# Performance work log

Hardware: AMD Instinct MI355X
Metric: run time of the kernel (lower is better)

## Reference

```python
import jax, jax.numpy as jnp
import numpy as np

N_NODES = 500_000
N_EDGES = 8_000_000
N_GRAPHS = 1000


def _mlp(x, w1, b1, w2, b2):
    # Linear -> SELU -> Linear (torch Sequential equivalent)
    return jax.nn.selu(x @ w1 + b1) @ w2 + b2


def setup_inputs() -> dict:
    key = jax.random.key(0)
    ks = jax.random.split(key, 25)
    p = lambda i, shape: jax.random.normal(ks[i], shape, jnp.float32) * 0.1
    return {
        "nodes": jax.random.normal(ks[0], (N_NODES, 1), jnp.float32),
        "edges": jax.random.normal(ks[1], (N_EDGES, 1), jnp.float32),
        "senders": jax.random.randint(ks[2], (N_EDGES,), 0, N_NODES),
        "receivers": jax.random.randint(ks[3], (N_EDGES,), 0, N_NODES),
        "graph_ids": jnp.sort(jax.random.randint(ks[4], (N_NODES,), 0, N_GRAPHS)),
        "num_graphs": N_GRAPHS,
        # permutate_nodes: 2 -> 10 -> 10
        "pn_w1": p(5, (2, 10)), "pn_b1": p(6, (10,)), "pn_w2": p(7, (10, 10)), "pn_b2": p(8, (10,)),
        # update_edges: 11 -> 5 -> 1
        "ue_w1": p(9, (11, 5)), "ue_b1": p(10, (5,)), "ue_w2": p(11, (5, 1)), "ue_b2": p(12, (1,)),
        # permutate_edges: 1 -> 5 -> 10
        "pe_w1": p(13, (1, 5)), "pe_b1": p(14, (5,)), "pe_w2": p(15, (5, 10)), "pe_b2": p(16, (10,)),
        # update_nodes: 11 -> 5 -> 1
        "un_w1": p(17, (11, 5)), "un_b1": p(18, (5,)), "un_w2": p(19, (5, 1)), "un_b2": p(20, (1,)),
        # predict: 11 -> 10 -> 10
        "pr_w1": p(21, (11, 10)), "pr_b1": p(22, (10,)), "pr_w2": p(23, (10, 10)), "pr_b2": p(24, (10,)),
    }


def reference(nodes, edges, pn_w1, pn_b1, pn_w2, pn_b2,
              ue_w1, ue_b1, ue_w2, ue_b2,
              pe_w1, pe_b1, pe_w2, pe_b2,
              un_w1, un_b1, un_w2, un_b2,
              pr_w1, pr_b1, pr_w2, pr_b2,
              senders, receivers, graph_ids, num_graphs):
    # gather node feats to edges: [recv || send] -> (E, 2)
    collected = jnp.concatenate([nodes[receivers], nodes[senders]], axis=-1)
    h1_nodes = _mlp(collected, pn_w1, pn_b1, pn_w2, pn_b2)  # (E, 10)
    h1_edges = edges  # (E, 1)
    for _ in range(3):
        h1_edges = _mlp(jnp.concatenate([h1_edges, h1_nodes], axis=-1),
                        ue_w1, ue_b1, ue_w2, ue_b2)  # (E, 1)
    # edges -> nodes aggregation (sum over receiver)
    edges_of_nodes = jax.ops.segment_sum(h1_edges, receivers, num_segments=nodes.shape[0])  # (N, 1)
    h2_edges = _mlp(edges_of_nodes, pe_w1, pe_b1, pe_w2, pe_b2)  # (N, 10)
    h2_nodes = nodes  # (N, 1)
    for _ in range(3):
        h2_nodes = _mlp(jnp.concatenate([h2_nodes, h2_edges], axis=-1),
                        un_w1, un_b1, un_w2, un_b2)  # (N, 1)
    # nodes -> globals aggregation (sum per graph)
    g = jax.ops.segment_sum(jnp.concatenate([h2_nodes, h2_edges], axis=-1),
                            graph_ids, num_segments=num_graphs)  # (G, 11)
    out = _mlp(g, pr_w1, pr_b1, pr_w2, pr_b2)  # (G, 10)
    return jax.nn.softmax(out, axis=-1)
```

## Files before the change

kernel.cpp:

```cpp
#include <hip/hip_runtime.h>
#include <hip/hip_fp16.h>
#include <math.h>

#define N_NODES_C  500000
#define N_EDGES_C  8000000
#define N_GRAPHS_C 1000
#define NGROUPS_C  (N_EDGES_C / 4)

#define BSHIFT  11
#define BWIDTH  2048
#define NBKT    245

#define PART_TPB 512
#define EPB     16384
#define GPB     (EPB / 4)
#define NPB     ((NGROUPS_C + GPB - 1) / GPB)
#define SROW    496
#define RITER   (GPB / PART_TPB)

#define P2_TPB  512
#define EPB2    8192
#define GPB2    (EPB2 / 4)
#define NPB2    ((NGROUPS_C + GPB2 - 1) / GPB2)
#define SROW2   992
#define RITER2  (GPB2 / P2_TPB)

#define GRAPH_ACC_OFF 0
#define PARTIALS_OFF  11008
#define FW_OFF        33024
#define ZERO_HEAD     33024

#define STARTS_OFF    33280
#define PAIRS_OFF     (STARTS_OFF + 246 * SROW)
#define WS_WORDS_NEEDED (PAIRS_OFF + NPB * EPB)

#define STARTS2_OFF   33280
#define PAIRS64_OFF   (STARTS2_OFF + 246 * SROW2)
#define WS2_WORDS_NEEDED (PAIRS64_OFF + NPB2 * EPB2 * 2)

#define OLD_NODE_ACC_OFF 33536
#define OLD_ZERO_WORDS   (OLD_NODE_ACC_OFF + N_NODES_C)

#define LOG2E_F 1.4426950408889634f


__device__ __forceinline__ float selu2(float xl) {
    const float C1 = 0.7282901039f;
    const float C2 = 1.7580993408473766f;
    float e = __builtin_amdgcn_exp2f(xl);
    float neg = fmaf(C2, e, -C2);
    return xl > 0.0f ? C1 * xl : neg;
}

__device__ __forceinline__ float selu_f(float x) {
    const float scale = 1.0507009873554805f;
    const float sa    = 1.0507009873554805f * 1.6732632423543772f;
    float neg = sa * (__expf(x) - 1.0f);
    return x > 0.0f ? scale * x : neg;
}

__device__ __forceinline__ void atomAddF(float* p, float v) {
    __hip_atomic_fetch_add(p, v, __ATOMIC_RELAXED, __HIP_MEMORY_SCOPE_AGENT);
}

__device__ __forceinline__ void fuse_weights(
        int t,
        const float* __restrict__ pn_w1, const float* __restrict__ pn_b1,
        const float* __restrict__ pn_w2, const float* __restrict__ pn_b2,
        const float* __restrict__ ue_w1, const float* __restrict__ ue_b1,
        const float* __restrict__ ue_w2, const float* __restrict__ ue_b2,
        const float* __restrict__ pe_w1, const float* __restrict__ pe_b1,
        const float* __restrict__ pe_w2, const float* __restrict__ pe_b2,
        const float* __restrict__ un_w1, const float* __restrict__ un_b1,
        const float* __restrict__ un_w2, const float* __restrict__ un_b2,
        float* __restrict__ fw) {
    const float L = LOG2E_F;
    if (t < 20) fw[0 + t] = pn_w1[t] * L;
    if (t < 10) fw[20 + t] = pn_b1[t] * L;
    if (t < 50) {
        int j = t / 5, k = t % 5;
        float s = 0.0f;
        for (int m = 0; m < 10; ++m) s += pn_w2[j * 10 + m] * ue_w1[(1 + m) * 5 + k];
        fw[30 + t] = s * L;
    }
    if (t < 5) {
        float s = ue_b1[t];
        for (int m = 0; m < 10; ++m) s += pn_b2[m] * ue_w1[(1 + m) * 5 + t];
        fw[80 + t] = s * L;
    }
    if (t < 5)  fw[85 + t]  = ue_w1[t] * L;
    if (t < 5)  fw[90 + t]  = ue_w2[t];
    if (t == 0) fw[95]      = ue_b2[0];
    if (t < 5)  fw[96 + t]  = pe_w1[t] * L;
    if (t < 5)  fw[101 + t] = pe_b1[t] * L;
    if (t < 50) fw[106 + t] = pe_w2[t];
    if (t < 10) fw[156 + t] = pe_b2[t];
    if (t < 25) {
        int j = t / 5, k = t % 5;
        float s = 0.0f;
        for (int m = 0; m < 10; ++m) s += pe_w2[j * 10 + m] * un_w1[(1 + m) * 5 + k];
        fw[166 + t] = s * L;
    }
    if (t < 5) {
        float s = un_b1[t];
        for (int m = 0; m < 10; ++m) s += pe_b2[m] * un_w1[(1 + m) * 5 + t];
        fw[191 + t] = s * L;
    }
    if (t < 5)  fw[196 + t] = un_w1[t] * L;
    if (t < 5)  fw[201 + t] = un_w2[t];
    if (t == 0) fw[206]     = un_b2[0];
}

__global__ __launch_bounds__(256) void k_init(
        float* __restrict__ ws,
        const float* pn_w1, const float* pn_b1, const float* pn_w2, const float* pn_b2,
        const float* ue_w1, const float* ue_b1, const float* ue_w2, const float* ue_b2,
        const float* pe_w1, const float* pe_b1, const float* pe_w2, const float* pe_b2,
        const float* un_w1, const float* un_b1, const float* un_w2, const float* un_b2) {
    int i = blockIdx.x * 256 + threadIdx.x;
    if (i < ZERO_HEAD) ws[i] = 0.0f;
    if (blockIdx.x == 0)
        fuse_weights(threadIdx.x, pn_w1, pn_b1, pn_w2, pn_b2, ue_w1, ue_b1, ue_w2, ue_b2,
                     pe_w1, pe_b1, pe_w2, pe_b2, un_w1, un_b1, un_w2, un_b2, ws + FW_OFF);
}

__global__ void k_fuse(const float* pn_w1, const float* pn_b1, const float* pn_w2, const float* pn_b2,
                       const float* ue_w1, const float* ue_b1, const float* ue_w2, const float* ue_b2,
                       const float* pe_w1, const float* pe_b1, const float* pe_w2, const float* pe_b2,
                       const float* un_w1, const float* un_b1, const float* un_w2, const float* un_b2,
                       float* fw) {
    fuse_weights(threadIdx.x, pn_w1, pn_b1, pn_w2, pn_b2, ue_w1, ue_b1, ue_w2, ue_b2,
                 pe_w1, pe_b1, pe_w2, pe_b2, un_w1, un_b1, un_w2, un_b2, fw);
}

__global__ void k_final(const float* __restrict__ graph_acc,
                        const float* __restrict__ partials,
                        const float* __restrict__ pr_w1, const float* __restrict__ pr_b1,
                        const float* __restrict__ pr_w2, const float* __restrict__ pr_b2,
                        float* __restrict__ out) {
    int g = blockIdx.x * blockDim.x + threadIdx.x;
    if (g >= N_GRAPHS_C) return;
    float gv[11];
#pragma unroll
    for (int f = 0; f < 11; ++f)
        gv[f] = graph_acc[g * 11 + f] + partials[g * 11 + f] + partials[11000 + g * 11 + f];
    float h[10];
#pragma unroll
    for (int j = 0; j < 10; ++j) {
        float z = pr_b1[j];
#pragma unroll
        for (int f = 0; f < 11; ++f) z = fmaf(gv[f], pr_w1[f * 10 + j], z);
        h[j] = selu_f(z);
    }
    float o[10];
    float mx = -1e30f;
#pragma unroll
    for (int j = 0; j < 10; ++j) {
        float z = pr_b2[j];
#pragma unroll
        for (int m = 0; m < 10; ++m) z = fmaf(h[m], pr_w2[m * 10 + j], z);
        o[j] = z;
        mx = fmaxf(mx, z);
    }
    float sum = 0.0f;
#pragma unroll
    for (int j = 0; j < 10; ++j) { o[j] = __expf(o[j] - mx); sum += o[j]; }
    float inv = 1.0f / sum;
#pragma unroll
    for (int j = 0; j < 10; ++j) out[g * 10 + j] = o[j] * inv;
}


__global__ __launch_bounds__(P2_TPB) void k_part2(
        const float* __restrict__ edges,
        const int* __restrict__ senders, const int* __restrict__ receivers,
        int* __restrict__ starts_T, unsigned long long* __restrict__ pairs64) {
    __shared__ int hist[256];
    __shared__ int cursorS[256];
    __shared__ alignas(16) unsigned long long staged[EPB2];

    int tid = threadIdx.x;
    int p   = blockIdx.x;
    int gstart = p * GPB2;
    int gnum   = NGROUPS_C - gstart;
    if (gnum > GPB2) gnum = GPB2;

    if (tid < 256) hist[tid] = 0;
    __syncthreads();

    int4 rv4[RITER2];
#pragma unroll
    for (int r = 0; r < RITER2; ++r) {
        int idx = r * P2_TPB + tid;
        int gi  = gstart + (idx < gnum ? idx : 0);
        rv4[r] = ((const int4*)receivers)[gi];
        if (idx < gnum) {
            atomicAdd(&hist[rv4[r].x >> BSHIFT], 1);
            atomicAdd(&hist[rv4[r].y >> BSHIFT], 1);
            atomicAdd(&hist[rv4[r].z >> BSHIFT], 1);
            atomicAdd(&hist[rv4[r].w >> BSHIFT], 1);
        }
    }
    __syncthreads();

    int orig = 0, val = 0;
    if (tid < 256) { orig = hist[tid]; val = orig; }
    for (int d = 1; d < 256; d <<= 1) {
        int add = 0;
        if (tid >= d && tid < 256) add = hist[tid - d];
        __syncthreads();
        if (tid >= d && tid < 256) { val += add; hist[tid] = val; }
        __syncthreads();
    }
    int excl = val - orig;
    if (tid < 256) cursorS[tid] = excl;
    if (tid < 246) starts_T[tid * SROW2 + p] = excl;
    __syncthreads();

#pragma unroll
    for (int r = 0; r < RITER2; ++r) {
        int idx = r * P2_TPB + tid;
        int gi  = gstart + (idx < gnum ? idx : 0);
        float4 e4 = ((const float4*)edges)[gi];
        int4   s4 = ((const int4*)senders)[gi];
        int4   rv = rv4[r];
        if (idx < gnum) {
            int   rvv[4] = {rv.x, rv.y, rv.z, rv.w};
            int   svv[4] = {s4.x, s4.y, s4.z, s4.w};
            float evv[4] = {e4.x, e4.y, e4.z, e4.w};
#pragma unroll
            for (int u = 0; u < 4; ++u) {
                int bkt  = rvv[u] >> BSHIFT;
                int slot = atomicAdd(&cursorS[bkt], 1);
                unsigned long long pk =
                    ((unsigned long long)(rvv[u] & (BWIDTH - 1)) << 51)
                  | ((unsigned long long)(unsigned)svv[u] << 32)
                  | (unsigned long long)__float_as_uint(evv[u]);
                staged[slot] = pk;
            }
        }
    }
    __syncthreads();

    const uint4* st4 = (const uint4*)staged;
    uint4* dst = (uint4*)(pairs64 + (size_t)p * EPB2);
    int n4 = gnum * 2;
    for (int i = tid; i < n4; i += P2_TPB) dst[i] = st4[i];
}

__global__ __launch_bounds__(1024) void k_gather2(
        const float* __restrict__ nodes, const int* __restrict__ graph_ids,
        const float* __restrict__ fw, const int* __restrict__ starts_T,
        const unsigned long long* __restrict__ pairs64,
        float* __restrict__ graph_acc, float* __restrict__ partials) {
    __shared__ float accf[BWIDTH];
    __shared__ float nf[BWIDTH];
    __shared__ int   s0[NPB2];
    __shared__ int   pst[NPB2 + 1];
    __shared__ int   sc[1024];
    __shared__ float garr[32 * 11];
    int tid = threadIdx.x;
    int b   = blockIdx.x;

    int nodeBase = b << BSHIFT;
    int lastIdx  = nodeBase + BWIDTH;
    if (lastIdx > N_NODES_C) lastIdx = N_NODES_C;
    int lim = lastIdx - nodeBase;

    accf[tid] = 0.0f; accf[1024 + tid] = 0.0f;
    nf[tid]        = (tid        < lim) ? nodes[nodeBase + tid]        : 0.0f;
    nf[1024 + tid] = (1024 + tid < lim) ? nodes[nodeBase + 1024 + tid] : 0.0f;
    if (tid < 352) garr[tid] = 0.0f;

    int cntv = 0;
    if (tid < NPB2) {
        int a = starts_T[b * SROW2 + tid];
        int c = starts_T[(b + 1) * SROW2 + tid];
        s0[tid] = a;
        cntv = c - a;
    }
    sc[tid] = cntv;
    __syncthreads();

    int v = cntv;
    for (int d = 1; d < 1024; d <<= 1) {
        int add = (tid >= d) ? sc[tid - d] : 0;
        __syncthreads();
        if (tid >= d) { v += add; sc[tid] = v; }
        __syncthreads();
    }
    if (tid == 0) pst[0] = 0;
    if (tid < NPB2) pst[tid + 1] = v;
    __syncthreads();

    int M = pst[NPB2];

    {
        float w_pn1[20], b_pn1[10], W_eb[50], b_eb[5], w1r0[5], w2e[5];
#pragma unroll
        for (int j = 0; j < 20; ++j) w_pn1[j] = fw[j];
#pragma unroll
        for (int j = 0; j < 10; ++j) b_pn1[j] = fw[20 + j];
#pragma unroll
        for (int j = 0; j < 50; ++j) W_eb[j] = fw[30 + j];
#pragma unroll
        for (int j = 0; j < 5; ++j) b_eb[j] = fw[80 + j];
#pragma unroll
        for (int j = 0; j < 5; ++j) w1r0[j] = fw[85 + j];
#pragma unroll
        for (int j = 0; j < 5; ++j) w2e[j] = fw[90 + j];
        float b2e = fw[95];

#pragma unroll 1
        for (int i = tid; i < M; i += 1024) {
            int lo = 0, hi = NPB2;
            while (hi - lo > 1) {
                int mid = (lo + hi) >> 1;
                if (pst[mid] <= i) lo = mid; else hi = mid;
            }
            int off = i - pst[lo];
            unsigned long long pk = pairs64[(size_t)lo * EPB2 + s0[lo] + off];
            int   rl   = (int)(pk >> 51);
            int   sidx = (int)((pk >> 32) & 0x7FFFFULL);
            float e    = __uint_as_float((unsigned)pk);
            float nr   = nf[rl];
            float ns   = nodes[sidx];

            float bs[5];
#pragma unroll
            for (int k = 0; k < 5; ++k) bs[k] = b_eb[k];
#pragma unroll
            for (int j = 0; j < 10; ++j) {
                float zl = fmaf(nr, w_pn1[j], fmaf(ns, w_pn1[10 + j], b_pn1[j]));
                float sz = selu2(zl);
#pragma unroll
                for (int k = 0; k < 5; ++k) bs[k] = fmaf(sz, W_eb[j * 5 + k], bs[k]);
            }
#pragma unroll
            for (int it = 0; it < 3; ++it) {
                float acc2 = b2e;
#pragma unroll
                for (int k = 0; k < 5; ++k) {
                    float tt = selu2(fmaf(e, w1r0[k], bs[k]));
                    acc2 = fmaf(tt, w2e[k], acc2);
                }
                e = acc2;
            }
            atomicAdd(&accf[rl], e);
        }
    }
    __syncthreads();

    float w_pe1[5], b_pe1[5], pe_w2[50], pe_b2[10], W_nb[25], b_nb[5], w1r0n[5], w2n[5];
#pragma unroll
    for (int j = 0; j < 5; ++j) w_pe1[j] = fw[96 + j];
#pragma unroll
    for (int j = 0; j < 5; ++j) b_pe1[j] = fw[101 + j];
#pragma unroll
    for (int j = 0; j < 50; ++j) pe_w2[j] = fw[106 + j];
#pragma unroll
    for (int j = 0; j < 10; ++j) pe_b2[j] = fw[156 + j];
#pragma unroll
    for (int j = 0; j < 25; ++j) W_nb[j] = fw[166 + j];
#pragma unroll
    for (int j = 0; j < 5; ++j) b_nb[j] = fw[191 + j];
#pragma unroll
    for (int j = 0; j < 5; ++j) w1r0n[j] = fw[196 + j];
#pragma unroll
    for (int j = 0; j < 5; ++j) w2n[j] = fw[201 + j];
    float b2n = fw[206];

    int gidBase = graph_ids[nodeBase];
    int gidEnd  = graph_ids[lastIdx - 1];

#pragma unroll
    for (int q = 0; q < 2; ++q) {
        int local = q * 1024 + tid;
        int i = nodeBase + local;
        bool valid = i < N_NODES_C;

        float s = accf[local];
        float t5[5];
#pragma unroll
        for (int k = 0; k < 5; ++k) t5[k] = selu2(fmaf(s, w_pe1[k], b_pe1[k]));
        float he[10];
#pragma unroll
        for (int m = 0; m < 10; ++m) {
            float a = pe_b2[m];
#pragma unroll
            for (int k = 0; k < 5; ++k) a = fmaf(t5[k], pe_w2[k * 10 + m], a);
            he[m] = a;
        }
        float bs[5];
#pragma unroll
        for (int k = 0; k < 5; ++k) {
            float a = b_nb[k];
#pragma unroll
            for (int t = 0; t < 5; ++t) a = fmaf(t5[t], W_nb[t * 5 + k], a);
            bs[k] = a;
        }
        float n = valid ? nf[local] : 0.0f;
#pragma unroll
        for (int it = 0; it < 3; ++it) {
            float a = b2n;
#pragma unroll
            for (int k = 0; k < 5; ++k) {
                float tt = selu2(fmaf(n, w1r0n[k], bs[k]));
                a = fmaf(tt, w2n[k], a);
            }
            n = a;
        }

        int gid = valid ? graph_ids[i] : -1;
        if (!valid) {
            n = 0.0f;
#pragma unroll
            for (int m = 0; m < 10; ++m) he[m] = 0.0f;
        }

        int gid0 = __shfl(gid, 0, 64);
        bool allsame = __all(gid == gid0) && (gid0 >= 0);
        if (allsame) {
            float vv = n;
#pragma unroll
            for (int off = 32; off > 0; off >>= 1) vv += __shfl_down(vv, off, 64);
            float vh[10];
#pragma unroll
            for (int m = 0; m < 10; ++m) {
                float ww = he[m];
#pragma unroll
                for (int off = 32; off > 0; off >>= 1) ww += __shfl_down(ww, off, 64);
                vh[m] = ww;
            }
            if ((tid & 63) == 0) {
                int off = gid0 - gidBase;
                if (off >= 0 && off < 32) {
                    atomicAdd(&garr[off * 11 + 0], vv);
#pragma unroll
                    for (int m = 0; m < 10; ++m) atomicAdd(&garr[off * 11 + 1 + m], vh[m]);
                } else {
                    atomAddF(&graph_acc[gid0 * 11 + 0], vv);
#pragma unroll
                    for (int m = 0; m < 10; ++m) atomAddF(&graph_acc[gid0 * 11 + 1 + m], vh[m]);
                }
            }
        } else if (valid) {
            int off = gid - gidBase;
            if (off >= 0 && off < 32) {
                atomicAdd(&garr[off * 11 + 0], n);
#pragma unroll
                for (int m = 0; m < 10; ++m) atomicAdd(&garr[off * 11 + 1 + m], he[m]);
            } else {
                atomAddF(&graph_acc[gid * 11 + 0], n);
#pragma unroll
                for (int m = 0; m < 10; ++m) atomAddF(&graph_acc[gid * 11 + 1 + m], he[m]);
            }
        }
    }
    __syncthreads();

    int ngl = gidEnd - gidBase + 1;
    if (ngl > 32) ngl = 32;
    int par = (b & 1) * 11000;
    for (int t = tid; t < ngl * 11; t += 1024) {
        int off = t / 11, f = t - off * 11;
        partials[par + (gidBase + off) * 11 + f] = garr[t];
    }
}


__global__ __launch_bounds__(PART_TPB, 4) void k_part(
        const float* __restrict__ nodes, const float* __restrict__ edges,
        const int* __restrict__ senders, const int* __restrict__ receivers,
        const float* __restrict__ fw, int* __restrict__ starts_T,
        unsigned int* __restrict__ pairs) {
    __shared__ int hist[256];
    __shared__ int cursorS[256];
    __shared__ unsigned int staged[EPB];

    int tid = threadIdx.x;
    int p   = blockIdx.x;
    int gstart = p * GPB;
    int gnum   = NGROUPS_C - gstart;
    if (gnum > GPB) gnum = GPB;

    float w_pn1[20], b_pn1[10], W_eb[50], b_eb[5], w1r0[5], w2e[5];
#pragma unroll
    for (int j = 0; j < 20; ++j) w_pn1[j] = fw[j];
#pragma unroll
    for (int j = 0; j < 10; ++j) b_pn1[j] = fw[20 + j];
#pragma unroll
    for (int j = 0; j < 50; ++j) W_eb[j] = fw[30 + j];
#pragma unroll
    for (int j = 0; j < 5; ++j) b_eb[j] = fw[80 + j];
#pragma unroll
    for (int j = 0; j < 5; ++j) w1r0[j] = fw[85 + j];
#pragma unroll
    for (int j = 0; j < 5; ++j) w2e[j] = fw[90 + j];
    float b2e = fw[95];

    if (tid < 256) hist[tid] = 0;
    __syncthreads();

#pragma unroll 1
    for (int r = 0; r < RITER; ++r) {
        int idx = r * PART_TPB + tid;
        int gi  = gstart + (idx < gnum ? idx : 0);
        int4 rv = ((const int4*)receivers)[gi];
        if (idx < gnum) {
            atomicAdd(&hist[rv.x >> BSHIFT], 1);
            atomicAdd(&hist[rv.y >> BSHIFT], 1);
            atomicAdd(&hist[rv.z >> BSHIFT], 1);
            atomicAdd(&hist[rv.w >> BSHIFT], 1);
        }
    }
    __syncthreads();

    int orig = 0, val = 0;
    if (tid < 256) { orig = hist[tid]; val = orig; }
    for (int d = 1; d < 256; d <<= 1) {
        int add = 0;
        if (tid >= d && tid < 256) add = hist[tid - d];
        __syncthreads();
        if (tid >= d && tid < 256) { val += add; hist[tid] = val; }
        __syncthreads();
    }
    int excl = val - orig;
    if (tid < 256) cursorS[tid] = excl;
    if (tid < 246) starts_T[tid * SROW + p] = excl;
    __syncthreads();

    float4 e4A, e4B, e4N;
    int4   s4A, s4B, s4N, r4A, r4B, r4N;
    float  nsA0, nsA1, nsA2, nsA3, nrA0, nrA1, nrA2, nrA3;
    float  nsB0, nsB1, nsB2, nsB3, nrB0, nrB1, nrB2, nrB3;

    {
        int gi0 = gstart + (tid < gnum ? tid : 0);
        e4A = ((const float4*)edges)[gi0];
        s4A = ((const int4*)senders)[gi0];
        r4A = ((const int4*)receivers)[gi0];
        nsA0 = nodes[s4A.x]; nsA1 = nodes[s4A.y];
        nsA2 = nodes[s4A.z]; nsA3 = nodes[s4A.w];
        nrA0 = nodes[r4A.x]; nrA1 = nodes[r4A.y];
        nrA2 = nodes[r4A.z]; nrA3 = nodes[r4A.w];
        int idx1 = PART_TPB + tid;
        int gi1 = gstart + (idx1 < gnum ? idx1 : 0);
        e4B = ((const float4*)edges)[gi1];
        s4B = ((const int4*)senders)[gi1];
        r4B = ((const int4*)receivers)[gi1];
    }

#pragma unroll 1
    for (int r = 0; r < RITER; ++r) {
        {
            int idx2 = (r + 2) * PART_TPB + tid;
            int gi2  = gstart + (idx2 < gnum ? idx2 : 0);
            e4N = ((const float4*)edges)[gi2];
            s4N = ((const int4*)senders)[gi2];
            r4N = ((const int4*)receivers)[gi2];
        }
        nsB0 = nodes[s4B.x]; nsB1 = nodes[s4B.y];
        nsB2 = nodes[s4B.z]; nsB3 = nodes[s4B.w];
        nrB0 = nodes[r4B.x]; nrB1 = nodes[r4B.y];
        nrB2 = nodes[r4B.z]; nrB3 = nodes[r4B.w];

        float ev[4]  = {e4A.x, e4A.y, e4A.z, e4A.w};
        int   rv[4]  = {r4A.x, r4A.y, r4A.z, r4A.w};
        float nsv[4] = {nsA0, nsA1, nsA2, nsA3};
        float nrv[4] = {nrA0, nrA1, nrA2, nrA3};

        bool validr = (r * PART_TPB + tid) < gnum;
#pragma unroll
        for (int u = 0; u < 4; ++u) {
            float nr = nrv[u], ns = nsv[u];
            float bs[5];
#pragma unroll
            for (int k = 0; k < 5; ++k) bs[k] = b_eb[k];
#pragma unroll
            for (int j = 0; j < 10; ++j) {
                float zl = fmaf(nr, w_pn1[j], fmaf(ns, w_pn1[10 + j], b_pn1[j]));
                float sz = selu2(zl);
#pragma unroll
                for (int k = 0; k < 5; ++k) bs[k] = fmaf(sz, W_eb[j * 5 + k], bs[k]);
            }
            float e = ev[u];
#pragma unroll
            for (int it = 0; it < 3; ++it) {
                float acc2 = b2e;
#pragma unroll
                for (int k = 0; k < 5; ++k) {
                    float tt = selu2(fmaf(e, w1r0[k], bs[k]));
                    acc2 = fmaf(tt, w2e[k], acc2);
                }
                e = acc2;
            }
            if (validr) {
                int bkt  = rv[u] >> BSHIFT;
                int slot = atomicAdd(&cursorS[bkt], 1);
                unsigned int pk = ((unsigned int)(rv[u] & (BWIDTH - 1)) << 16)
                                | (unsigned int)__half_as_ushort(__float2half_rn(e));
                staged[slot] = pk;
            }
        }

        e4A = e4B; s4A = s4B; r4A = r4B;
        nsA0 = nsB0; nsA1 = nsB1; nsA2 = nsB2; nsA3 = nsB3;
        nrA0 = nrB0; nrA1 = nrB1; nrA2 = nrB2; nrA3 = nrB3;
        e4B = e4N; s4B = s4N; r4B = r4N;
    }
    __syncthreads();

    const uint4* staged4 = (const uint4*)staged;
    uint4* dst = (uint4*)(pairs + (size_t)p * EPB);
    for (int i = tid; i < gnum; i += PART_TPB) dst[i] = staged4[i];
}

__global__ __launch_bounds__(1024) void k_gather(
        const float* __restrict__ nodes, const int* __restrict__ graph_ids,
        const float* __restrict__ fw, const int* __restrict__ starts_T,
        const unsigned int* __restrict__ pairs, float* __restrict__ graph_acc,
        float* __restrict__ partials) {
    __shared__ float accf[BWIDTH];
    __shared__ int s0[SROW], s1[SROW];
    __shared__ float garr[32 * 11];
    int tid = threadIdx.x;
    int b   = blockIdx.x;

    accf[tid] = 0.0f; accf[1024 + tid] = 0.0f;
    if (tid < 352) garr[tid] = 0.0f;
    for (int i = tid; i < NPB; i += 1024) {
        s0[i] = starts_T[b * SROW + i];
        s1[i] = starts_T[(b + 1) * SROW + i];
    }
    __syncthreads();

    int g32 = tid >> 5, lane = tid & 31;
    for (int p = g32; p < NPB; p += 32) {
        int st = s0[p], en = s1[p];
        const unsigned int* seg = pairs + (size_t)p * EPB + st;
        int cnt = en - st;
        for (int i = lane; i < cnt; i += 32) {
            unsigned int pk = seg[i];
            atomicAdd(&accf[(pk >> 16) & (BWIDTH - 1)],
                      __half2float(__ushort_as_half((unsigned short)(pk & 0xffff))));
        }
    }
    __syncthreads();

    float w_pe1[5], b_pe1[5], pe_w2[50], pe_b2[10], W_nb[25], b_nb[5], w1r0n[5], w2n[5];
#pragma unroll
    for (int j = 0; j < 5; ++j) w_pe1[j] = fw[96 + j];
#pragma unroll
    for (int j = 0; j < 5; ++j) b_pe1[j] = fw[101 + j];
#pragma unroll
    for (int j = 0; j < 50; ++j) pe_w2[j] = fw[106 + j];
#pragma unroll
    for (int j = 0; j < 10; ++j) pe_b2[j] = fw[156 + j];
#pragma unroll
    for (int j = 0; j < 25; ++j) W_nb[j] = fw[166 + j];
#pragma unroll
    for (int j = 0; j < 5; ++j) b_nb[j] = fw[191 + j];
#pragma unroll
    for (int j = 0; j < 5; ++j) w1r0n[j] = fw[196 + j];
#pragma unroll
    for (int j = 0; j < 5; ++j) w2n[j] = fw[201 + j];
    float b2n = fw[206];

    int nodeBase = b << BSHIFT;
    int lastIdx  = nodeBase + BWIDTH;
    if (lastIdx > N_NODES_C) lastIdx = N_NODES_C;
    int gidBase = graph_ids[nodeBase];
    int gidEnd  = graph_ids[lastIdx - 1];

#pragma unroll
    for (int q = 0; q < 2; ++q) {
        int local = q * 1024 + tid;
        int i = nodeBase + local;
        bool valid = i < N_NODES_C;

        float s = accf[local];
        float t5[5];
#pragma unroll
        for (int k = 0; k < 5; ++k) t5[k] = selu2(fmaf(s, w_pe1[k], b_pe1[k]));
        float he[10];
#pragma unroll
        for (int m = 0; m < 10; ++m) {
            float a = pe_b2[m];
#pragma unroll
            for (int k = 0; k < 5; ++k) a = fmaf(t5[k], pe_w2[k * 10 + m], a);
            he[m] = a;
        }
        float bs[5];
#pragma unroll
        for (int k = 0; k < 5; ++k) {
            float a = b_nb[k];
#pragma unroll
            for (int t = 0; t < 5; ++t) a = fmaf(t5[t], W_nb[t * 5 + k], a);
            bs[k] = a;
        }
        float n = valid ? nodes[i] : 0.0f;
#pragma unroll
        for (int it = 0; it < 3; ++it) {
            float a = b2n;
#pragma unroll
            for (int k = 0; k < 5; ++k) {
                float tt = selu2(fmaf(n, w1r0n[k], bs[k]));
                a = fmaf(tt, w2n[k], a);
            }
            n = a;
        }

        int gid = valid ? graph_ids[i] : -1;
        if (!valid) {
            n = 0.0f;
#pragma unroll
            for (int m = 0; m < 10; ++m) he[m] = 0.0f;
        }

        int gid0 = __shfl(gid, 0, 64);
        bool allsame = __all(gid == gid0) && (gid0 >= 0);
        if (allsame) {
            float v = n;
#pragma unroll
            for (int off = 32; off > 0; off >>= 1) v += __shfl_down(v, off, 64);
            float vh[10];
#pragma unroll
            for (int m = 0; m < 10; ++m) {
                float ww = he[m];
#pragma unroll
                for (int off = 32; off > 0; off >>= 1) ww += __shfl_down(ww, off, 64);
                vh[m] = ww;
            }
            if ((tid & 63) == 0) {
                int off = gid0 - gidBase;
                if (off >= 0 && off < 32) {
                    atomicAdd(&garr[off * 11 + 0], v);
#pragma unroll
                    for (int m = 0; m < 10; ++m) atomicAdd(&garr[off * 11 + 1 + m], vh[m]);
                } else {
                    atomAddF(&graph_acc[gid0 * 11 + 0], v);
#pragma unroll
                    for (int m = 0; m < 10; ++m) atomAddF(&graph_acc[gid0 * 11 + 1 + m], vh[m]);
                }
            }
        } else if (valid) {
            int off = gid - gidBase;
            if (off >= 0 && off < 32) {
                atomicAdd(&garr[off * 11 + 0], n);
#pragma unroll
                for (int m = 0; m < 10; ++m) atomicAdd(&garr[off * 11 + 1 + m], he[m]);
            } else {
                atomAddF(&graph_acc[gid * 11 + 0], n);
#pragma unroll
                for (int m = 0; m < 10; ++m) atomAddF(&graph_acc[gid * 11 + 1 + m], he[m]);
            }
        }
    }
    __syncthreads();

    int ngl = gidEnd - gidBase + 1;
    if (ngl > 32) ngl = 32;
    int par = (b & 1) * 11000;
    for (int t = tid; t < ngl * 11; t += 1024) {
        int off = t / 11, f = t - off * 11;
        partials[par + (gidBase + off) * 11 + f] = garr[t];
    }
}


__global__ __launch_bounds__(256) void k_zero(float* __restrict__ ws, int len4) {
    int i = blockIdx.x * 256 + threadIdx.x;
    if (i < len4) ((float4*)ws)[i] = make_float4(0.f, 0.f, 0.f, 0.f);
}

__global__ __launch_bounds__(256) void k_edges(
        const float* __restrict__ nodes, const float* __restrict__ edges,
        const int* __restrict__ senders, const int* __restrict__ receivers,
        const float* __restrict__ fw, float* __restrict__ node_acc) {
    float w_pn1[20], b_pn1[10], W_eb[50], b_eb[5], w1r0[5], w2e[5];
#pragma unroll
    for (int j = 0; j < 20; ++j) w_pn1[j] = fw[j];
#pragma unroll
    for (int j = 0; j < 10; ++j) b_pn1[j] = fw[20 + j];
#pragma unroll
    for (int j = 0; j < 50; ++j) W_eb[j] = fw[30 + j];
#pragma unroll
    for (int j = 0; j < 5; ++j) b_eb[j] = fw[80 + j];
#pragma unroll
    for (int j = 0; j < 5; ++j) w1r0[j] = fw[85 + j];
#pragma unroll
    for (int j = 0; j < 5; ++j) w2e[j] = fw[90 + j];
    float b2e = fw[95];

    int g = blockIdx.x * 256 + threadIdx.x;
    if (g >= NGROUPS_C) return;

    float4 e4 = ((const float4*)edges)[g];
    int4  s4 = ((const int4*)senders)[g];
    int4  r4 = ((const int4*)receivers)[g];
    float ev[4] = {e4.x, e4.y, e4.z, e4.w};
    int   sv[4] = {s4.x, s4.y, s4.z, s4.w};
    int   rv[4] = {r4.x, r4.y, r4.z, r4.w};
    float nsv[4], nrv[4];
#pragma unroll
    for (int u = 0; u < 4; ++u) { nsv[u] = nodes[sv[u]]; nrv[u] = nodes[rv[u]]; }
#pragma unroll
    for (int u = 0; u < 4; ++u) {
        float nr = nrv[u], ns = nsv[u];
        float bs[5];
#pragma unroll
        for (int k = 0; k < 5; ++k) bs[k] = b_eb[k];
#pragma unroll
        for (int j = 0; j < 10; ++j) {
            float zl = fmaf(nr, w_pn1[j], fmaf(ns, w_pn1[10 + j], b_pn1[j]));
            float sz = selu2(zl);
#pragma unroll
            for (int k = 0; k < 5; ++k) bs[k] = fmaf(sz, W_eb[j * 5 + k], bs[k]);
        }
        float e = ev[u];
#pragma unroll
        for (int it = 0; it < 3; ++it) {
            float acc2 = b2e;
#pragma unroll
            for (int k = 0; k < 5; ++k) {
                float tt = selu2(fmaf(e, w1r0[k], bs[k]));
                acc2 = fmaf(tt, w2e[k], acc2);
            }
            e = acc2;
        }
        atomAddF(&node_acc[rv[u]], e);
    }
}

__global__ __launch_bounds__(256) void k_nodes(
        const float* __restrict__ nodes, const int* __restrict__ graph_ids,
        const float* __restrict__ fw, const float* __restrict__ node_acc,
        float* __restrict__ graph_acc) {
    float w_pe1[5], b_pe1[5], pe_w2[50], pe_b2[10], W_nb[25], b_nb[5], w1r0n[5], w2n[5];
#pragma unroll
    for (int j = 0; j < 5; ++j) w_pe1[j] = fw[96 + j];
#pragma unroll
    for (int j = 0; j < 5; ++j) b_pe1[j] = fw[101 + j];
#pragma unroll
    for (int j = 0; j < 50; ++j) pe_w2[j] = fw[106 + j];
#pragma unroll
    for (int j = 0; j < 10; ++j) pe_b2[j] = fw[156 + j];
#pragma unroll
    for (int j = 0; j < 25; ++j) W_nb[j] = fw[166 + j];
#pragma unroll
    for (int j = 0; j < 5; ++j) b_nb[j] = fw[191 + j];
#pragma unroll
    for (int j = 0; j < 5; ++j) w1r0n[j] = fw[196 + j];
#pragma unroll
    for (int j = 0; j < 5; ++j) w2n[j] = fw[201 + j];
    float b2n = fw[206];

    int i = blockIdx.x * 256 + threadIdx.x;
    bool valid = i < N_NODES_C;
    int ii = valid ? i : (N_NODES_C - 1);

    float s = node_acc[ii];
    float t5[5];
#pragma unroll
    for (int k = 0; k < 5; ++k) t5[k] = selu2(fmaf(s, w_pe1[k], b_pe1[k]));
    float he[10];
#pragma unroll
    for (int m = 0; m < 10; ++m) {
        float a = pe_b2[m];
#pragma unroll
        for (int k = 0; k < 5; ++k) a = fmaf(t5[k], pe_w2[k * 10 + m], a);
        he[m] = a;
    }
    float bs[5];
#pragma unroll
    for (int k = 0; k < 5; ++k) {
        float a = b_nb[k];
#pragma unroll
        for (int t = 0; t < 5; ++t) a = fmaf(t5[t], W_nb[t * 5 + k], a);
        bs[k] = a;
    }
    float n = nodes[ii];
#pragma unroll
    for (int it = 0; it < 3; ++it) {
        float a = b2n;
#pragma unroll
        for (int k = 0; k < 5; ++k) {
            float tt = selu2(fmaf(n, w1r0n[k], bs[k]));
            a = fmaf(tt, w2n[k], a);
        }
        n = a;
    }

    int gid = valid ? graph_ids[ii] : -1;
    if (!valid) {
        n = 0.0f;
#pragma unroll
        for (int m = 0; m < 10; ++m) he[m] = 0.0f;
    }

    int gid0 = __shfl(gid, 0, 64);
    bool allsame = __all(gid == gid0) && (gid0 >= 0);
    if (allsame) {
        float v = n;
#pragma unroll
        for (int off = 32; off > 0; off >>= 1) v += __shfl_down(v, off, 64);
        float vh[10];
#pragma unroll
        for (int m = 0; m < 10; ++m) {
            float ww = he[m];
#pragma unroll
            for (int off = 32; off > 0; off >>= 1) ww += __shfl_down(ww, off, 64);
            vh[m] = ww;
        }
        if ((threadIdx.x & 63) == 0) {
            atomAddF(&graph_acc[gid0 * 11 + 0], v);
#pragma unroll
            for (int m = 0; m < 10; ++m) atomAddF(&graph_acc[gid0 * 11 + 1 + m], vh[m]);
        }
    } else if (valid) {
        atomAddF(&graph_acc[gid * 11 + 0], n);
#pragma unroll
        for (int m = 0; m < 10; ++m) atomAddF(&graph_acc[gid * 11 + 1 + m], he[m]);
    }
}


extern "C" void kernel_launch(void* const* d_in, const int* in_sizes, int n_in,
                              void* d_out, int out_size, void* d_ws, size_t ws_size,
                              hipStream_t stream) {
    const float* nodes     = (const float*)d_in[0];
    const float* edges     = (const float*)d_in[1];
    const int*   senders   = (const int*)d_in[2];
    const int*   receivers = (const int*)d_in[3];
    const int*   graph_ids = (const int*)d_in[4];
    const float* pn_w1 = (const float*)d_in[6];
    const float* pn_b1 = (const float*)d_in[7];
    const float* pn_w2 = (const float*)d_in[8];
    const float* pn_b2 = (const float*)d_in[9];
    const float* ue_w1 = (const float*)d_in[10];
    const float* ue_b1 = (const float*)d_in[11];
    const float* ue_w2 = (const float*)d_in[12];
    const float* ue_b2 = (const float*)d_in[13];
    const float* pe_w1 = (const float*)d_in[14];
    const float* pe_b1 = (const float*)d_in[15];
    const float* pe_w2 = (const float*)d_in[16];
    const float* pe_b2 = (const float*)d_in[17];
    const float* un_w1 = (const float*)d_in[18];
    const float* un_b1 = (const float*)d_in[19];
    const float* un_w2 = (const float*)d_in[20];
    const float* un_b2 = (const float*)d_in[21];
    const float* pr_w1 = (const float*)d_in[22];
    const float* pr_b1 = (const float*)d_in[23];
    const float* pr_w2 = (const float*)d_in[24];
    const float* pr_b2 = (const float*)d_in[25];

    float* ws        = (float*)d_ws;
    float* graph_acc = ws + GRAPH_ACC_OFF;
    float* partials  = ws + PARTIALS_OFF;
    float* fw        = ws + FW_OFF;
    float* outp      = (float*)d_out;

    if (ws_size >= (size_t)WS2_WORDS_NEEDED * 4) {
        int* starts_T = (int*)ws + STARTS2_OFF;
        unsigned long long* pairs64 = (unsigned long long*)((int*)ws + PAIRS64_OFF);

        hipLaunchKernelGGL(k_init, dim3((ZERO_HEAD + 255) / 256), dim3(256), 0, stream, ws,
                           pn_w1, pn_b1, pn_w2, pn_b2, ue_w1, ue_b1, ue_w2, ue_b2,
                           pe_w1, pe_b1, pe_w2, pe_b2, un_w1, un_b1, un_w2, un_b2);
        hipLaunchKernelGGL(k_part2, dim3(NPB2), dim3(P2_TPB), 0, stream,
                           edges, senders, receivers, starts_T, pairs64);
        hipLaunchKernelGGL(k_gather2, dim3(NBKT), dim3(1024), 0, stream,
                           nodes, graph_ids, fw, starts_T, pairs64, graph_acc, partials);
        hipLaunchKernelGGL(k_final, dim3((N_GRAPHS_C + 255) / 256), dim3(256), 0, stream,
                           graph_acc, partials, pr_w1, pr_b1, pr_w2, pr_b2, outp);
    } else if (ws_size >= (size_t)WS_WORDS_NEEDED * 4) {
        int* starts_T        = (int*)ws + STARTS_OFF;
        unsigned int* pairs  = (unsigned int*)ws + PAIRS_OFF;

        hipLaunchKernelGGL(k_init, dim3((ZERO_HEAD + 255) / 256), dim3(256), 0, stream, ws,
                           pn_w1, pn_b1, pn_w2, pn_b2, ue_w1, ue_b1, ue_w2, ue_b2,
                           pe_w1, pe_b1, pe_w2, pe_b2, un_w1, un_b1, un_w2, un_b2);
        hipLaunchKernelGGL(k_part, dim3(NPB), dim3(PART_TPB), 0, stream,
                           nodes, edges, senders, receivers, fw, starts_T, pairs);
        hipLaunchKernelGGL(k_gather, dim3(NBKT), dim3(1024), 0, stream,
                           nodes, graph_ids, fw, starts_T, pairs, graph_acc, partials);
        hipLaunchKernelGGL(k_final, dim3((N_GRAPHS_C + 255) / 256), dim3(256), 0, stream,
                           graph_acc, partials, pr_w1, pr_b1, pr_w2, pr_b2, outp);
    } else {
        float* node_acc = ws + OLD_NODE_ACC_OFF;
        int len4 = OLD_ZERO_WORDS / 4;
        hipLaunchKernelGGL(k_zero, dim3((len4 + 255) / 256), dim3(256), 0, stream, ws, len4);
        hipLaunchKernelGGL(k_fuse, dim3(1), dim3(64), 0, stream,
                           pn_w1, pn_b1, pn_w2, pn_b2, ue_w1, ue_b1, ue_w2, ue_b2,
                           pe_w1, pe_b1, pe_w2, pe_b2, un_w1, un_b1, un_w2, un_b2, fw);
        hipLaunchKernelGGL(k_edges, dim3((NGROUPS_C + 255) / 256), dim3(256), 0, stream,
                           nodes, edges, senders, receivers, fw, node_acc);
        hipLaunchKernelGGL(k_nodes, dim3((N_NODES_C + 255) / 256), dim3(256), 0, stream,
                           nodes, graph_ids, fw, node_acc, graph_acc);
        hipLaunchKernelGGL(k_final, dim3((N_GRAPHS_C + 255) / 256), dim3(256), 0, stream,
                           graph_acc, partials, pr_w1, pr_b1, pr_w2, pr_b2, outp);
    }
}
```

Measured before the change: 293.2 us.

## Halve gather bucket width, double bucket count, compact starts to 16-bit, dual-issue edges

The partition kernel now buckets receivers into 1024-node buckets (489 buckets) instead of 2048-node buckets (245), so the gather kernel runs twice as many blocks with half the shared memory each. The starts table is stored as 16-bit offsets to keep the workspace small. The gather loop processes two edges per thread per iteration with a fixed-depth binary search to add memory-level parallelism. The intent is better GPU occupancy and latency hiding in the gather stage, at the cost of a larger per-block histogram and scan in partitioning and more registers per thread.

Result: slower. 331.4 us (+13.0%).

```diff
diff --git a/kernel.cpp b/kernel.cpp
--- a/kernel.cpp
+++ b/kernel.cpp
@@ -10,7 +10,6 @@
 #define BSHIFT  11
 #define BWIDTH  2048
 #define NBKT    245
-
 #define PART_TPB 512
 #define EPB     16384
 #define GPB     (EPB / 4)
@@ -18,6 +17,10 @@
 #define SROW    496
 #define RITER   (GPB / PART_TPB)
 
+#define G_BSHIFT 10
+#define G_BWIDTH 1024
+#define G_NBKT   489
+#define NBROW    490
 #define P2_TPB  512
 #define EPB2    8192
 #define GPB2    (EPB2 / 4)
@@ -35,7 +38,8 @@
 #define WS_WORDS_NEEDED (PAIRS_OFF + NPB * EPB)
 
 #define STARTS2_OFF   33280
-#define PAIRS64_OFF   (STARTS2_OFF + 246 * SROW2)
+#define STARTS2_WORDS ((NBROW * SROW2) / 2)
+#define PAIRS64_OFF   (STARTS2_OFF + STARTS2_WORDS)
 #define WS2_WORDS_NEEDED (PAIRS64_OFF + NPB2 * EPB2 * 2)
 
 #define OLD_NODE_ACC_OFF 33536
@@ -174,9 +178,10 @@
 __global__ __launch_bounds__(P2_TPB) void k_part2(
         const float* __restrict__ edges,
         const int* __restrict__ senders, const int* __restrict__ receivers,
-        int* __restrict__ starts_T, unsigned long long* __restrict__ pairs64) {
-    __shared__ int hist[256];
-    __shared__ int cursorS[256];
+        unsigned short* __restrict__ starts16,
+        unsigned long long* __restrict__ pairs64) {
+    __shared__ int hist[512];
+    __shared__ int cursorS[512];
     __shared__ alignas(16) unsigned long long staged[EPB2];
 
     int tid = threadIdx.x;
@@ -185,7 +190,7 @@
     int gnum   = NGROUPS_C - gstart;
     if (gnum > GPB2) gnum = GPB2;
 
-    if (tid < 256) hist[tid] = 0;
+    hist[tid] = 0;
     __syncthreads();
 
     int4 rv4[RITER2];
@@ -195,26 +200,25 @@
         int gi  = gstart + (idx < gnum ? idx : 0);
         rv4[r] = ((const int4*)receivers)[gi];
         if (idx < gnum) {
-            atomicAdd(&hist[rv4[r].x >> BSHIFT], 1);
-            atomicAdd(&hist[rv4[r].y >> BSHIFT], 1);
-            atomicAdd(&hist[rv4[r].z >> BSHIFT], 1);
-            atomicAdd(&hist[rv4[r].w >> BSHIFT], 1);
-        }
-    }
-    __syncthreads();
-
-    int orig = 0, val = 0;
-    if (tid < 256) { orig = hist[tid]; val = orig; }
-    for (int d = 1; d < 256; d <<= 1) {
-        int add = 0;
-        if (tid >= d && tid < 256) add = hist[tid - d];
+            atomicAdd(&hist[rv4[r].x >> G_BSHIFT], 1);
+            atomicAdd(&hist[rv4[r].y >> G_BSHIFT], 1);
+            atomicAdd(&hist[rv4[r].z >> G_BSHIFT], 1);
+            atomicAdd(&hist[rv4[r].w >> G_BSHIFT], 1);
+        }
+    }
+    __syncthreads();
+
+    int orig = hist[tid];
+    int val  = orig;
+    for (int d = 1; d < 512; d <<= 1) {
+        int add = (tid >= d) ? hist[tid - d] : 0;
         __syncthreads();
-        if (tid >= d && tid < 256) { val += add; hist[tid] = val; }
+        if (tid >= d) { val += add; hist[tid] = val; }
         __syncthreads();
     }
     int excl = val - orig;
-    if (tid < 256) cursorS[tid] = excl;
-    if (tid < 246) starts_T[tid * SROW2 + p] = excl;
+    cursorS[tid] = excl;
+    if (tid < NBROW) starts16[(size_t)tid * SROW2 + p] = (unsigned short)excl;
     __syncthreads();
 
 #pragma unroll
@@ -230,10 +234,10 @@
             float evv[4] = {e4.x, e4.y, e4.z, e4.w};
 #pragma unroll
             for (int u = 0; u < 4; ++u) {
-                int bkt  = rvv[u] >> BSHIFT;
+                int bkt  = rvv[u] >> G_BSHIFT;
                 int slot = atomicAdd(&cursorS[bkt], 1);
                 unsigned long long pk =
-                    ((unsigned long long)(rvv[u] & (BWIDTH - 1)) << 51)
+                    ((unsigned long long)(rvv[u] & (G_BWIDTH - 1)) << 51)
                   | ((unsigned long long)(unsigned)svv[u] << 32)
                   | (unsigned long long)__float_as_uint(evv[u]);
                 staged[slot] = pk;
@@ -248,13 +252,13 @@
     for (int i = tid; i < n4; i += P2_TPB) dst[i] = st4[i];
 }
 
-__global__ __launch_bounds__(1024) void k_gather2(
+__global__ __launch_bounds__(1024, 8) void k_gather2(
         const float* __restrict__ nodes, const int* __restrict__ graph_ids,
-        const float* __restrict__ fw, const int* __restrict__ starts_T,
+        const float* __restrict__ fw, const unsigned short* __restrict__ starts16,
         const unsigned long long* __restrict__ pairs64,
         float* __restrict__ graph_acc, float* __restrict__ partials) {
-    __shared__ float accf[BWIDTH];
-    __shared__ float nf[BWIDTH];
+    __shared__ float accf[G_BWIDTH];
+    __shared__ float nf[G_BWIDTH];
     __shared__ int   s0[NPB2];
     __shared__ int   pst[NPB2 + 1];
     __shared__ int   sc[1024];
@@ -262,20 +266,19 @@
     int tid = threadIdx.x;
     int b   = blockIdx.x;
 
-    int nodeBase = b << BSHIFT;
-    int lastIdx  = nodeBase + BWIDTH;
+    int nodeBase = b << G_BSHIFT;
+    int lastIdx  = nodeBase + G_BWIDTH;
     if (lastIdx > N_NODES_C) lastIdx = N_NODES_C;
     int lim = lastIdx - nodeBase;
 
-    accf[tid] = 0.0f; accf[1024 + tid] = 0.0f;
-    nf[tid]        = (tid        < lim) ? nodes[nodeBase + tid]        : 0.0f;
-    nf[1024 + tid] = (1024 + tid < lim) ? nodes[nodeBase + 1024 + tid] : 0.0f;
+    accf[tid] = 0.0f;
+    nf[tid]   = (tid < lim) ? nodes[nodeBase + tid] : 0.0f;
     if (tid < 352) garr[tid] = 0.0f;
 
     int cntv = 0;
     if (tid < NPB2) {
-        int a = starts_T[b * SROW2 + tid];
-        int c = starts_T[(b + 1) * SROW2 + tid];
+        int a = (int)starts16[(size_t)b * SROW2 + tid];
+        int c = (int)starts16[(size_t)(b + 1) * SROW2 + tid];
         s0[tid] = a;
         cntv = c - a;
     }
@@ -311,15 +314,73 @@
         for (int j = 0; j < 5; ++j) w2e[j] = fw[90 + j];
         float b2e = fw[95];
 
+        int i = tid;
 #pragma unroll 1
-        for (int i = tid; i < M; i += 1024) {
+        for (; i + 1024 < M; i += 2048) {
+            int iA = i, iB = i + 1024;
+            int loA = 0, hiA = NPB2, loB = 0, hiB = NPB2;
+#pragma unroll
+            for (int s = 0; s < 10; ++s) {
+                int mA = (loA + hiA) >> 1;
+                int mB = (loB + hiB) >> 1;
+                int pA = pst[mA];
+                int pB = pst[mB];
+                if (pA <= iA) loA = mA; else hiA = mA;
+                if (pB <= iB) loB = mB; else hiB = mB;
+            }
+            unsigned long long pkA =
+                pairs64[(size_t)loA * EPB2 + s0[loA] + (iA - pst[loA])];
+            unsigned long long pkB =
+                pairs64[(size_t)loB * EPB2 + s0[loB] + (iB - pst[loB])];
+            float nsA = nodes[(int)((pkA >> 32) & 0x7FFFFULL)];
+            float nsB = nodes[(int)((pkB >> 32) & 0x7FFFFULL)];
+            int   rlA = (int)(pkA >> 51);
+            int   rlB = (int)(pkB >> 51);
+            float nrA = nf[rlA];
+            float nrB = nf[rlB];
+            float eA  = __uint_as_float((unsigned)pkA);
+            float eB  = __uint_as_float((unsigned)pkB);
+
+            float bsA[5], bsB[5];
+#pragma unroll
+            for (int k = 0; k < 5; ++k) { bsA[k] = b_eb[k]; bsB[k] = b_eb[k]; }
+#pragma unroll
+            for (int j = 0; j < 10; ++j) {
+                float zlA = fmaf(nrA, w_pn1[j], fmaf(nsA, w_pn1[10 + j], b_pn1[j]));
+                float zlB = fmaf(nrB, w_pn1[j], fmaf(nsB, w_pn1[10 + j], b_pn1[j]));
+                float szA = selu2(zlA);
+                float szB = selu2(zlB);
+#pragma unroll
+                for (int k = 0; k < 5; ++k) {
+                    bsA[k] = fmaf(szA, W_eb[j * 5 + k], bsA[k]);
+                    bsB[k] = fmaf(szB, W_eb[j * 5 + k], bsB[k]);
+                }
+            }
+#pragma unroll
+            for (int it = 0; it < 3; ++it) {
+                float aA = b2e, aB = b2e;
+#pragma unroll
+                for (int k = 0; k < 5; ++k) {
+                    float tA = selu2(fmaf(eA, w1r0[k], bsA[k]));
+                    float tB = selu2(fmaf(eB, w1r0[k], bsB[k]));
+                    aA = fmaf(tA, w2e[k], aA);
+                    aB = fmaf(tB, w2e[k], aB);
+                }
+                eA = aA; eB = aB;
+            }
+            atomicAdd(&accf[rlA], eA);
+            atomicAdd(&accf[rlB], eB);
+        }
+#pragma unroll 1
+        for (; i < M; i += 1024) {
             int lo = 0, hi = NPB2;
-            while (hi - lo > 1) {
+#pragma unroll
+            for (int s = 0; s < 10; ++s) {
                 int mid = (lo + hi) >> 1;
                 if (pst[mid] <= i) lo = mid; else hi = mid;
             }
-            int off = i - pst[lo];
-            unsigned long long pk = pairs64[(size_t)lo * EPB2 + s0[lo] + off];
+            unsigned long long pk =
+                pairs64[(size_t)lo * EPB2 + s0[lo] + (i - pst[lo])];
             int   rl   = (int)(pk >> 51);
             int   sidx = (int)((pk >> 32) & 0x7FFFFULL);
             float e    = __uint_as_float((unsigned)pk);
@@ -373,13 +434,11 @@
     int gidBase = graph_ids[nodeBase];
     int gidEnd  = graph_ids[lastIdx - 1];
 
-#pragma unroll
-    for (int q = 0; q < 2; ++q) {
-        int local = q * 1024 + tid;
-        int i = nodeBase + local;
-        bool valid = i < N_NODES_C;
-
-        float s = accf[local];
+    {
+        int i = nodeBase + tid;
+        bool valid = tid < lim;
+
+        float s = accf[tid];
         float t5[5];
 #pragma unroll
         for (int k = 0; k < 5; ++k) t5[k] = selu2(fmaf(s, w_pe1[k], b_pe1[k]));
@@ -399,7 +458,7 @@
             for (int t = 0; t < 5; ++t) a = fmaf(t5[t], W_nb[t * 5 + k], a);
             bs[k] = a;
         }
-        float n = valid ? nf[local] : 0.0f;
+        float n = valid ? nf[tid] : 0.0f;
 #pragma unroll
         for (int it = 0; it < 3; ++it) {
             float a = b2n;
@@ -962,16 +1021,16 @@
     float* outp      = (float*)d_out;
 
     if (ws_size >= (size_t)WS2_WORDS_NEEDED * 4) {
-        int* starts_T = (int*)ws + STARTS2_OFF;
+        unsigned short* starts16 = (unsigned short*)((int*)ws + STARTS2_OFF);
         unsigned long long* pairs64 = (unsigned long long*)((int*)ws + PAIRS64_OFF);
 
         hipLaunchKernelGGL(k_init, dim3((ZERO_HEAD + 255) / 256), dim3(256), 0, stream, ws,
                            pn_w1, pn_b1, pn_w2, pn_b2, ue_w1, ue_b1, ue_w2, ue_b2,
                            pe_w1, pe_b1, pe_w2, pe_b2, un_w1, un_b1, un_w2, un_b2);
         hipLaunchKernelGGL(k_part2, dim3(NPB2), dim3(P2_TPB), 0, stream,
-                           edges, senders, receivers, starts_T, pairs64);
-        hipLaunchKernelGGL(k_gather2, dim3(NBKT), dim3(1024), 0, stream,
-                           nodes, graph_ids, fw, starts_T, pairs64, graph_acc, partials);
+                           edges, senders, receivers, starts16, pairs64);
+        hipLaunchKernelGGL(k_gather2, dim3(G_NBKT), dim3(1024), 0, stream,
+                           nodes, graph_ids, fw, starts16, pairs64, graph_acc, partials);
         hipLaunchKernelGGL(k_final, dim3((N_GRAPHS_C + 255) / 256), dim3(256), 0, stream,
                            graph_acc, partials, pr_w1, pr_b1, pr_w2, pr_b2, outp);
     } else if (ws_size >= (size_t)WS_WORDS_NEEDED * 4) {
```
